# Performance work log

Measured on AMD Instinct MI355X. Metric: run time of the kernel, lower is better.

The kernel has to match this reference:

```python
import jax, jax.numpy as jnp
import numpy as np

D = 1024       # dim
RATIO = 8
H = 4          # num_heads
HD = D // RATIO // H   # head_dim = 32
INNER = H * HD         # 128
SQ, SK, N = 2048, 2048, 8


def _xavier(k, shape):
    fan_out, fan_in = shape
    lim = float(np.sqrt(6.0 / (fan_in + fan_out)))
    return jax.random.uniform(k, shape, jnp.float32, -lim, lim)


def setup_inputs() -> dict:
    key = jax.random.key(0)
    ks = jax.random.split(key, 6)
    query = jax.random.normal(ks[0], (SQ, N, D), jnp.float32)
    key_feat = jax.random.normal(ks[1], (SK, N, D), jnp.float32)
    Wq = _xavier(ks[2], (INNER, D))
    Wk = _xavier(ks[3], (INNER, D))
    Wv = _xavier(ks[4], (INNER, D))
    Wup = _xavier(ks[5], (D, INNER))
    return {"query": query, "key_feat": key_feat, "Wq": Wq, "Wk": Wk, "Wv": Wv, "Wup": Wup}


def reference(query, key_feat, Wq, Wk, Wv, Wup):
    # query: (Sq, N, D), key_feat: (Sk, N, D); Conv1d with kernel 1 == per-position linear
    scale = HD ** -0.5
    n = query.shape[1]
    # project and reshape to (N, H, head_dim, seq) matching Conv1d output view
    q = jnp.einsum('snd,ed->nes', query, Wq).reshape(n, H, HD, SQ)
    k = jnp.einsum('snd,ed->nes', key_feat, Wk).reshape(n, H, HD, SK)
    v = jnp.einsum('snd,ed->nes', key_feat, Wv).reshape(n, H, HD, SK)
    # attn = q^T @ k * scale -> (N, H, Sq, Sk)
    attn = jnp.einsum('nhcp,nhck->nhpk', q, k) * scale
    attn = jax.nn.softmax(attn, axis=-1)
    # x = attn @ v^T -> (N, H, Sq, head_dim)
    x = jnp.einsum('nhpk,nhck->nhpc', attn, v)
    # permute(0,2,1,3).view(N, Sq, INNER)
    x = x.transpose(0, 2, 1, 3).reshape(n, SQ, INNER)
    # up-projection then permute(2,0,1) -> (Sq, N, D)
    out = jnp.einsum('npe,de->pnd', x, Wup)
    return out
```

## Files before the change

### kernel.cpp

```cpp
#include <hip/hip_runtime.h>

typedef unsigned int uint;
typedef unsigned short ushort;
typedef float f32x4 __attribute__((ext_vector_type(4)));
typedef short bf16x8 __attribute__((ext_vector_type(8)));

#define SQ_   2048
#define SK_   2048
#define NB    8
#define DD    1024
#define INNER 128
#define H_    4
#define HD    32
#define ALPHA 0.17677669529663687f
#define PROW  136

__device__ __forceinline__ ushort f2bf(float f) {
    uint u = __float_as_uint(f);
    u += 0x7fffu + ((u >> 16) & 1u);
    return (ushort)(u >> 16);
}
__device__ __forceinline__ uint pack2(float a, float b) {
    return (uint)f2bf(a) | ((uint)f2bf(b) << 16);
}

__global__ __launch_bounds__(256) void wprep_kernel(
    const float* __restrict__ Wq, const float* __restrict__ Wk,
    const float* __restrict__ Wv, const float* __restrict__ Wup,
    ushort* __restrict__ wbf, ushort* __restrict__ wup_bf)
{
    int idx = (blockIdx.x * 256 + threadIdx.x) * 8;
    const float* W;
    ushort* dst;
    float sc = 1.0f;
    int off;
    if (idx < 393216) {
        int which = idx >> 17;
        off = idx & 131071;
        W = (which == 0) ? Wq : (which == 1) ? Wk : Wv;
        if (which == 0) sc = ALPHA;
        dst = wbf + idx;
    } else {
        off = idx - 393216;
        W = Wup;
        dst = wup_bf + off;
    }
    float4 a = *(const float4*)(W + off);
    float4 b = *(const float4*)(W + off + 4);
    uint4 o;
    o.x = pack2(a.x * sc, a.y * sc);
    o.y = pack2(a.z * sc, a.w * sc);
    o.z = pack2(b.x * sc, b.y * sc);
    o.w = pack2(b.z * sc, b.w * sc);
    *(uint4*)dst = o;
}

__global__ __launch_bounds__(256) void proj_mfma(
    const float* __restrict__ query, const float* __restrict__ key_feat,
    const ushort* __restrict__ wbf,
    ushort* __restrict__ q_ws, ushort* __restrict__ k_ws, ushort* __restrict__ v_ws)
{
    const int which = blockIdx.y;
    const float* src = (which == 0) ? query : key_feat;
    const ushort* W  = wbf + (size_t)which * (INNER * DD);
    ushort* dst      = (which == 0) ? q_ws : (which == 1) ? k_ws : v_ws;

    __shared__ ushort Xs[64 * PROW];

    const int pblk = blockIdx.x;
    const int t = threadIdx.x;
    const int wave = t >> 6, lane = t & 63, quad = lane >> 4, col = lane & 15;

    const int sp = t >> 2, sq = t & 3;
    const float* srow = src + (size_t)(pblk * 64 + sp) * DD + sq * 32;
    ushort* lrow = Xs + sp * PROW + sq * 32;

    f32x4 acc[2][4];
#pragma unroll
    for (int e = 0; e < 2; e++)
#pragma unroll
        for (int pt = 0; pt < 4; pt++) acc[e][pt] = (f32x4){0.f, 0.f, 0.f, 0.f};

    const ushort* wrow0 = W + (size_t)(32 * wave + col) * DD + quad * 8;
    const ushort* wrow1 = W + (size_t)(32 * wave + 16 + col) * DD + quad * 8;

    for (int slab = 0; slab < DD / 128; slab++) {
        const float4* g = (const float4*)(srow + slab * 128);
        float4 f0 = g[0], f1 = g[1], f2 = g[2], f3 = g[3];
        float4 f4 = g[4], f5 = g[5], f6 = g[6], f7 = g[7];
        __syncthreads();
        uint4 u;
        u.x = pack2(f0.x, f0.y); u.y = pack2(f0.z, f0.w);
        u.z = pack2(f1.x, f1.y); u.w = pack2(f1.z, f1.w);
        *(uint4*)(lrow) = u;
        u.x = pack2(f2.x, f2.y); u.y = pack2(f2.z, f2.w);
        u.z = pack2(f3.x, f3.y); u.w = pack2(f3.z, f3.w);
        *(uint4*)(lrow + 8) = u;
        u.x = pack2(f4.x, f4.y); u.y = pack2(f4.z, f4.w);
        u.z = pack2(f5.x, f5.y); u.w = pack2(f5.z, f5.w);
        *(uint4*)(lrow + 16) = u;
        u.x = pack2(f6.x, f6.y); u.y = pack2(f6.z, f6.w);
        u.z = pack2(f7.x, f7.y); u.w = pack2(f7.z, f7.w);
        *(uint4*)(lrow + 24) = u;
        __syncthreads();

#pragma unroll
        for (int kk = 0; kk < 4; kk++) {
            bf16x8 aW0 = *(const bf16x8*)(wrow0 + slab * 128 + kk * 32);
            bf16x8 aW1 = *(const bf16x8*)(wrow1 + slab * 128 + kk * 32);
#pragma unroll
            for (int pt = 0; pt < 4; pt++) {
                bf16x8 bX = *(const bf16x8*)(Xs + (pt * 16 + col) * PROW + kk * 32 + quad * 8);
                acc[0][pt] = __builtin_amdgcn_mfma_f32_16x16x32_bf16(aW0, bX, acc[0][pt], 0, 0, 0);
                acc[1][pt] = __builtin_amdgcn_mfma_f32_16x16x32_bf16(aW1, bX, acc[1][pt], 0, 0, 0);
            }
        }
    }

#pragma unroll
    for (int pt = 0; pt < 4; pt++) {
        int p = pblk * 64 + pt * 16 + col;
        int s = p >> 3, n = p & 7;
        ushort* base = dst + ((size_t)(n * H_ + wave) * 2048 + s) * HD;
#pragma unroll
        for (int e = 0; e < 2; e++) {
            uint2 pk;
            pk.x = pack2(acc[e][pt][0], acc[e][pt][1]);
            pk.y = pack2(acc[e][pt][2], acc[e][pt][3]);
            *(uint2*)(base + e * 16 + quad * 4) = pk;
        }
    }
}

__global__ __launch_bounds__(256) void vtrans_kernel(
    const ushort* __restrict__ v_ws, ushort* __restrict__ vt_ws)
{
    const int nh = blockIdx.x >> 4;
    const int slab = blockIdx.x & 15;
    __shared__ ushort t[HD][132];
    const uint* src = (const uint*)(v_ws + ((size_t)nh * SK_ + slab * 128) * HD);
#pragma unroll
    for (int it = 0; it < 8; it++) {
        int i = it * 256 + threadIdx.x;
        int key = i >> 4, j = i & 15;
        uint u = src[i];
        t[2 * j][key]     = (ushort)(u & 0xffffu);
        t[2 * j + 1][key] = (ushort)(u >> 16);
    }
    __syncthreads();
    uint* dst = (uint*)vt_ws;
#pragma unroll
    for (int it = 0; it < 8; it++) {
        int i = it * 256 + threadIdx.x;
        int c = i >> 6, kk = (i & 63) * 2;
        dst[(size_t)(nh * HD + c) * (SK_ / 2) + slab * 64 + (i & 63)] =
            (uint)t[c][kk] | ((uint)t[c][kk + 1] << 16);
    }
}

__global__ __launch_bounds__(256) void attn_mfma(
    const ushort* __restrict__ q_ws, const ushort* __restrict__ k_ws,
    const ushort* __restrict__ vt_ws, ushort* __restrict__ x_ws)
{
    const int nh   = blockIdx.y;
    const int lane = threadIdx.x & 63;
    const int wave = threadIdx.x >> 6;
    const int quad = lane >> 4;
    const int col  = lane & 15;
    const int qbase = blockIdx.x * 64 + wave * 16;

    const bf16x8 bQ = *(const bf16x8*)(q_ws + ((size_t)nh * SQ_ + qbase + col) * HD + quad * 8);

    f32x4 acc0 = {0.f, 0.f, 0.f, 0.f};
    f32x4 acc1 = {0.f, 0.f, 0.f, 0.f};
    float lsum = 0.f;

    const ushort* kb = k_ws  + (size_t)nh * SK_ * HD;
    const ushort* vb = vt_ws + (size_t)nh * HD * SK_;
    const int sA = ((quad & 1) << 5) + col;
    const int sB = sA + 16;
    const bool lo = quad < 2;

#pragma unroll 2
    for (int kc = 0; kc < SK_; kc += 32) {
        bf16x8 aK0 = *(const bf16x8*)(kb + (size_t)(kc + col) * HD + quad * 8);
        bf16x8 aK1 = *(const bf16x8*)(kb + (size_t)(kc + 16 + col) * HD + quad * 8);
        bf16x8 aV0 = *(const bf16x8*)(vb + (size_t)col * SK_ + kc + quad * 8);
        bf16x8 aV1 = *(const bf16x8*)(vb + (size_t)(col + 16) * SK_ + kc + quad * 8);

        f32x4 z = {0.f, 0.f, 0.f, 0.f};
        f32x4 s0 = __builtin_amdgcn_mfma_f32_16x16x32_bf16(aK0, bQ, z, 0, 0, 0);
        f32x4 s1 = __builtin_amdgcn_mfma_f32_16x16x32_bf16(aK1, bQ, z, 0, 0, 0);

        float p00 = __expf(s0[0]), p01 = __expf(s0[1]), p02 = __expf(s0[2]), p03 = __expf(s0[3]);
        float p10 = __expf(s1[0]), p11 = __expf(s1[1]), p12 = __expf(s1[2]), p13 = __expf(s1[3]);
        lsum += ((p00 + p01) + (p02 + p03)) + ((p10 + p11) + (p12 + p13));

        uint t0A = pack2(p00, p01), t0B = pack2(p02, p03);
        uint t1A = pack2(p10, p11), t1B = pack2(p12, p13);

        int y0 = __shfl((int)t0A, sA, 64), y1 = __shfl((int)t1A, sA, 64);
        int y2 = __shfl((int)t0B, sA, 64), y3 = __shfl((int)t1B, sA, 64);
        int y4 = __shfl((int)t0A, sB, 64), y5 = __shfl((int)t1A, sB, 64);
        int y6 = __shfl((int)t0B, sB, 64), y7 = __shfl((int)t1B, sB, 64);
        uint4 bp;
        bp.x = lo ? (uint)y0 : (uint)y1;
        bp.y = lo ? (uint)y2 : (uint)y3;
        bp.z = lo ? (uint)y4 : (uint)y5;
        bp.w = lo ? (uint)y6 : (uint)y7;
        bf16x8 bP = __builtin_bit_cast(bf16x8, bp);

        acc0 = __builtin_amdgcn_mfma_f32_16x16x32_bf16(aV0, bP, acc0, 0, 0, 0);
        acc1 = __builtin_amdgcn_mfma_f32_16x16x32_bf16(aV1, bP, acc1, 0, 0, 0);
    }

    lsum += __shfl_xor(lsum, 16, 64);
    lsum += __shfl_xor(lsum, 32, 64);
    const float inv = 1.f / lsum;

    const int n = nh >> 2, h = nh & 3;
    ushort* xo = x_ws + ((size_t)n * SQ_ + qbase + col) * INNER + h * HD;
    uint2 pk0, pk1;
    pk0.x = pack2(acc0[0] * inv, acc0[1] * inv);
    pk0.y = pack2(acc0[2] * inv, acc0[3] * inv);
    pk1.x = pack2(acc1[0] * inv, acc1[1] * inv);
    pk1.y = pack2(acc1[2] * inv, acc1[3] * inv);
    *(uint2*)(xo + quad * 4)      = pk0;
    *(uint2*)(xo + 16 + quad * 4) = pk1;
}

__global__ __launch_bounds__(256) void up_mfma(
    const ushort* __restrict__ x_ws, const ushort* __restrict__ wup_bf,
    float* __restrict__ out)
{
    const int pblk = blockIdx.x;
    const int dblk = blockIdx.y;
    const int wave = threadIdx.x >> 6, lane = threadIdx.x & 63;
    const int quad = lane >> 4, col = lane & 15;

    const int p0 = pblk * 64 + wave * 16;
    const ushort* xrow = x_ws + (size_t)(p0 + col) * INNER + quad * 8;
    bf16x8 bX[4];
#pragma unroll
    for (int kk = 0; kk < 4; kk++)
        bX[kk] = *(const bf16x8*)(xrow + kk * 32);

    const int p = p0 + col;
    const int n = p >> 11, s = p & 2047;
    float* obase = out + ((size_t)s * NB + n) * DD;

#pragma unroll
    for (int mt = 0; mt < 4; mt++) {
        const int d0 = dblk * 64 + mt * 16;
        const ushort* wrow = wup_bf + (size_t)(d0 + col) * INNER + quad * 8;
        f32x4 acc = {0.f, 0.f, 0.f, 0.f};
#pragma unroll
        for (int kk = 0; kk < 4; kk++) {
            bf16x8 aW = *(const bf16x8*)(wrow + kk * 32);
            acc = __builtin_amdgcn_mfma_f32_16x16x32_bf16(aW, bX[kk], acc, 0, 0, 0);
        }
        *(float4*)(obase + d0 + quad * 4) = make_float4(acc[0], acc[1], acc[2], acc[3]);
    }
}

extern "C" void kernel_launch(void* const* d_in, const int* in_sizes, int n_in,
                              void* d_out, int out_size, void* d_ws, size_t ws_size,
                              hipStream_t stream)
{
    const float* query    = (const float*)d_in[0];
    const float* key_feat = (const float*)d_in[1];
    const float* Wq  = (const float*)d_in[2];
    const float* Wk  = (const float*)d_in[3];
    const float* Wv  = (const float*)d_in[4];
    const float* Wup = (const float*)d_in[5];
    float* out = (float*)d_out;

    ushort* ws16 = (ushort*)d_ws;
    const size_t SZ = (size_t)NB * H_ * 2048 * HD;
    ushort* q_ws   = ws16;
    ushort* k_ws   = ws16 + SZ;
    ushort* v_ws   = ws16 + 2 * SZ;
    ushort* vt_ws  = ws16 + 3 * SZ;
    ushort* wbf    = vt_ws;
    ushort* x_ws   = ws16 + 4 * SZ;
    ushort* wup_bf = ws16 + 5 * SZ;

    wprep_kernel<<<256, 256, 0, stream>>>(Wq, Wk, Wv, Wup, wbf, wup_bf);
    proj_mfma<<<dim3(256, 3), 256, 0, stream>>>(query, key_feat, wbf,
                                                q_ws, k_ws, v_ws);
    vtrans_kernel<<<512, 256, 0, stream>>>(v_ws, vt_ws);
    attn_mfma<<<dim3(32, 32), 256, 0, stream>>>(q_ws, k_ws, vt_ws, x_ws);
    up_mfma<<<dim3(256, 16), 256, 0, stream>>>(x_ws, wup_bf, out);
}
```

Before: 331.6 us.

## Rewrite attention core with 32x32 MFMA, exp2, permlane swap and split-K waves

The attention kernel now uses 32x32x16 bf16 MFMA tiles instead of 16x16x32. Each pair of waves splits the key range in half and combines partial accumulators and row sums through shared memory. The softmax scale folds in log2(e) so a raw v_exp_f32 replaces __expf, and hardware bf16 pack plus permlane32_swap replace software rounding and eight shuffles per step. This is meant to cut VALU and shuffle overhead in the inner loop, at the cost of an LDS reduction, a block barrier and half the waves idling during the epilogue.

```diff
diff --git a/kernel.cpp b/kernel.cpp
--- a/kernel.cpp
+++ b/kernel.cpp
@@ -3,6 +3,7 @@
 typedef unsigned int uint;
 typedef unsigned short ushort;
 typedef float f32x4 __attribute__((ext_vector_type(4)));
+typedef float f32x16 __attribute__((ext_vector_type(16)));
 typedef short bf16x8 __attribute__((ext_vector_type(8)));
 
 #define SQ_   2048
@@ -12,7 +13,7 @@
 #define INNER 128
 #define H_    4
 #define HD    32
-#define ALPHA 0.17677669529663687f
+#define ALPHA (0.17677669529663687f * 1.4426950408889634f)
 #define PROW  136
 
 __device__ __forceinline__ ushort f2bf(float f) {
@@ -22,6 +23,25 @@
 }
 __device__ __forceinline__ uint pack2(float a, float b) {
     return (uint)f2bf(a) | ((uint)f2bf(b) << 16);
+}
+__device__ __forceinline__ uint cvtpk(float a, float b) {
+    uint r;
+    asm("v_cvt_pk_bf16_f32 %0, %1, %2" : "=v"(r) : "v"(a), "v"(b));
+    return r;
+}
+__device__ __forceinline__ float fexp2(float x) {
+    float r;
+    asm("v_exp_f32 %0, %1" : "=v"(r) : "v"(x));
+    return r;
+}
+__device__ __forceinline__ void plswap(uint &a, uint &b) {
+#if __has_builtin(__builtin_amdgcn_permlane32_swap)
+    auto r = __builtin_amdgcn_permlane32_swap(a, b, false, false);
+    a = (uint)r[0];
+    b = (uint)r[1];
+#else
+    asm("v_permlane32_swap_b32 %0, %1" : "+v"(a), "+v"(b));
+#endif
 }
 
 __global__ __launch_bounds__(256) void wprep_kernel(
@@ -162,71 +182,84 @@
     const ushort* __restrict__ q_ws, const ushort* __restrict__ k_ws,
     const ushort* __restrict__ vt_ws, ushort* __restrict__ x_ws)
 {
-    const int nh   = blockIdx.y;
-    const int lane = threadIdx.x & 63;
-    const int wave = threadIdx.x >> 6;
-    const int quad = lane >> 4;
-    const int col  = lane & 15;
-    const int qbase = blockIdx.x * 64 + wave * 16;
-
-    const bf16x8 bQ = *(const bf16x8*)(q_ws + ((size_t)nh * SQ_ + qbase + col) * HD + quad * 8);
-
-    f32x4 acc0 = {0.f, 0.f, 0.f, 0.f};
-    f32x4 acc1 = {0.f, 0.f, 0.f, 0.f};
+    const int nh    = blockIdx.y;
+    const int lane  = threadIdx.x & 63;
+    const int wave  = threadIdx.x >> 6;
+    const int tile  = wave >> 1;
+    const int khalf = wave & 1;
+    const int row   = lane & 31;
+    const int hi    = lane >> 5;
+    const int qbase = blockIdx.x * 64 + tile * 32;
+
+    const ushort* qrow = q_ws + ((size_t)nh * SQ_ + qbase + row) * HD;
+    const bf16x8 bQ0 = *(const bf16x8*)(qrow + hi * 8);
+    const bf16x8 bQ1 = *(const bf16x8*)(qrow + 16 + hi * 8);
+
+    const ushort* kb = k_ws  + (size_t)nh * SK_ * HD + (size_t)row * HD + hi * 8;
+    const ushort* vb = vt_ws + (size_t)nh * HD * SK_ + (size_t)row * SK_ + hi * 8;
+
+    f32x16 acc = {};
     float lsum = 0.f;
 
-    const ushort* kb = k_ws  + (size_t)nh * SK_ * HD;
-    const ushort* vb = vt_ws + (size_t)nh * HD * SK_;
-    const int sA = ((quad & 1) << 5) + col;
-    const int sB = sA + 16;
-    const bool lo = quad < 2;
-
+    const int kc0 = khalf * (SK_ / 2);
 #pragma unroll 2
-    for (int kc = 0; kc < SK_; kc += 32) {
-        bf16x8 aK0 = *(const bf16x8*)(kb + (size_t)(kc + col) * HD + quad * 8);
-        bf16x8 aK1 = *(const bf16x8*)(kb + (size_t)(kc + 16 + col) * HD + quad * 8);
-        bf16x8 aV0 = *(const bf16x8*)(vb + (size_t)col * SK_ + kc + quad * 8);
-        bf16x8 aV1 = *(const bf16x8*)(vb + (size_t)(col + 16) * SK_ + kc + quad * 8);
-
-        f32x4 z = {0.f, 0.f, 0.f, 0.f};
-        f32x4 s0 = __builtin_amdgcn_mfma_f32_16x16x32_bf16(aK0, bQ, z, 0, 0, 0);
-        f32x4 s1 = __builtin_amdgcn_mfma_f32_16x16x32_bf16(aK1, bQ, z, 0, 0, 0);
-
-        float p00 = __expf(s0[0]), p01 = __expf(s0[1]), p02 = __expf(s0[2]), p03 = __expf(s0[3]);
-        float p10 = __expf(s1[0]), p11 = __expf(s1[1]), p12 = __expf(s1[2]), p13 = __expf(s1[3]);
-        lsum += ((p00 + p01) + (p02 + p03)) + ((p10 + p11) + (p12 + p13));
-
-        uint t0A = pack2(p00, p01), t0B = pack2(p02, p03);
-        uint t1A = pack2(p10, p11), t1B = pack2(p12, p13);
-
-        int y0 = __shfl((int)t0A, sA, 64), y1 = __shfl((int)t1A, sA, 64);
-        int y2 = __shfl((int)t0B, sA, 64), y3 = __shfl((int)t1B, sA, 64);
-        int y4 = __shfl((int)t0A, sB, 64), y5 = __shfl((int)t1A, sB, 64);
-        int y6 = __shfl((int)t0B, sB, 64), y7 = __shfl((int)t1B, sB, 64);
-        uint4 bp;
-        bp.x = lo ? (uint)y0 : (uint)y1;
-        bp.y = lo ? (uint)y2 : (uint)y3;
-        bp.z = lo ? (uint)y4 : (uint)y5;
-        bp.w = lo ? (uint)y6 : (uint)y7;
-        bf16x8 bP = __builtin_bit_cast(bf16x8, bp);
-
-        acc0 = __builtin_amdgcn_mfma_f32_16x16x32_bf16(aV0, bP, acc0, 0, 0, 0);
-        acc1 = __builtin_amdgcn_mfma_f32_16x16x32_bf16(aV1, bP, acc1, 0, 0, 0);
-    }
-
-    lsum += __shfl_xor(lsum, 16, 64);
-    lsum += __shfl_xor(lsum, 32, 64);
-    const float inv = 1.f / lsum;
-
-    const int n = nh >> 2, h = nh & 3;
-    ushort* xo = x_ws + ((size_t)n * SQ_ + qbase + col) * INNER + h * HD;
-    uint2 pk0, pk1;
-    pk0.x = pack2(acc0[0] * inv, acc0[1] * inv);
-    pk0.y = pack2(acc0[2] * inv, acc0[3] * inv);
-    pk1.x = pack2(acc1[0] * inv, acc1[1] * inv);
-    pk1.y = pack2(acc1[2] * inv, acc1[3] * inv);
-    *(uint2*)(xo + quad * 4)      = pk0;
-    *(uint2*)(xo + 16 + quad * 4) = pk1;
+    for (int kc = kc0; kc < kc0 + SK_ / 2; kc += 32) {
+        bf16x8 aK0 = *(const bf16x8*)(kb + (size_t)kc * HD);
+        bf16x8 aK1 = *(const bf16x8*)(kb + (size_t)kc * HD + 16);
+        bf16x8 aV0 = *(const bf16x8*)(vb + kc);
+        bf16x8 aV1 = *(const bf16x8*)(vb + kc + 16);
+
+        f32x16 S = {};
+        S = __builtin_amdgcn_mfma_f32_32x32x16_bf16(aK0, bQ0, S, 0, 0, 0);
+        S = __builtin_amdgcn_mfma_f32_32x32x16_bf16(aK1, bQ1, S, 0, 0, 0);
+
+        float p[16];
+#pragma unroll
+        for (int r = 0; r < 16; r++) p[r] = fexp2(S[r]);
+
+        lsum += ((((p[0] + p[1]) + (p[2] + p[3])) + ((p[4] + p[5]) + (p[6] + p[7])))
+               + (((p[8] + p[9]) + (p[10] + p[11])) + ((p[12] + p[13]) + (p[14] + p[15]))));
+
+        uint w0 = cvtpk(p[0], p[1]),   w2 = cvtpk(p[4], p[5]);
+        uint w1 = cvtpk(p[2], p[3]),   w3 = cvtpk(p[6], p[7]);
+        plswap(w0, w2);
+        plswap(w1, w3);
+        uint w4 = cvtpk(p[8], p[9]),   w6 = cvtpk(p[12], p[13]);
+        uint w5 = cvtpk(p[10], p[11]), w7 = cvtpk(p[14], p[15]);
+        plswap(w4, w6);
+        plswap(w5, w7);
+        bf16x8 bP0 = __builtin_bit_cast(bf16x8, make_uint4(w0, w1, w2, w3));
+        bf16x8 bP1 = __builtin_bit_cast(bf16x8, make_uint4(w4, w5, w6, w7));
+
+        acc = __builtin_amdgcn_mfma_f32_32x32x16_bf16(aV0, bP0, acc, 0, 0, 0);
+        acc = __builtin_amdgcn_mfma_f32_32x32x16_bf16(aV1, bP1, acc, 0, 0, 0);
+    }
+
+    __shared__ float red[2][16][64];
+    __shared__ float redl[2][64];
+    if (khalf) {
+#pragma unroll
+        for (int r = 0; r < 16; r++) red[tile][r][lane] = acc[r];
+        redl[tile][lane] = lsum;
+    }
+    __syncthreads();
+    if (!khalf) {
+#pragma unroll
+        for (int r = 0; r < 16; r++) acc[r] += red[tile][r][lane];
+        lsum += redl[tile][lane];
+        lsum += __shfl_xor(lsum, 32, 64);
+        const float inv = 1.f / lsum;
+
+        const int n = nh >> 2, h = nh & 3;
+        ushort* xo = x_ws + ((size_t)n * SQ_ + qbase + row) * INNER + h * HD;
+#pragma unroll
+        for (int rg = 0; rg < 4; rg++) {
+            uint2 pk;
+            pk.x = cvtpk(acc[rg * 4 + 0] * inv, acc[rg * 4 + 1] * inv);
+            pk.y = cvtpk(acc[rg * 4 + 2] * inv, acc[rg * 4 + 3] * inv);
+            *(uint2*)(xo + rg * 8 + hi * 4) = pk;
+        }
+    }
 }
 
 __global__ __launch_bounds__(256) void up_mfma(
@@ -289,6 +322,6 @@
     proj_mfma<<<dim3(256, 3), 256, 0, stream>>>(query, key_feat, wbf,
                                                 q_ws, k_ws, v_ws);
     vtrans_kernel<<<512, 256, 0, stream>>>(v_ws, vt_ws);
-    attn_mfma<<<dim3(32, 32), 256, 0, stream>>>(q_ws, k_ws, vt_ws, x_ws);
+    attn_mfma<<<dim3(SQ_ / 64, 32), 256, 0, stream>>>(q_ws, k_ws, vt_ws, x_ws);
     up_mfma<<<dim3(256, 16), 256, 0, stream>>>(x_ws, wup_bf, out);
 }
```

Result: faster. 289.5 us (-12.7%).
